# Kernel tuning notes

Hardware: AMD Instinct MI355X
Metric: run time of the kernel (lower is better)

The kernel has to match this reference:

```python
import jax, jax.numpy as jnp
import numpy as np

B, N, H = 32, 2048, 128
L4H = 4 * H  # concatenated (c0,h0,c1,h1) embedding dim


def _lstm_cell(x, c, h, Wx, Wh, b):
    g = x @ Wx + h @ Wh + b                      # [B,N,4H]
    i, f, gg, o = jnp.split(g, 4, axis=-1)
    c_new = jax.nn.sigmoid(f) * c + jax.nn.sigmoid(i) * jnp.tanh(gg)
    h_new = jax.nn.sigmoid(o) * jnp.tanh(c_new)
    return c_new, h_new


def setup_inputs() -> dict:
    key = jax.random.key(0)
    ks = jax.random.split(key, 20)
    s = 0.05
    inp = {
        'node_embeddings': jax.random.normal(ks[0], (B, N, H), jnp.float32),
        'c0': jax.random.normal(ks[1], (B, N, H), jnp.float32),
        'h0': jax.random.normal(ks[2], (B, N, H), jnp.float32),
        'c1': jax.random.normal(ks[3], (B, N, H), jnp.float32),
        'h1': jax.random.normal(ks[4], (B, N, H), jnp.float32),
        'instruction_pointer': jax.random.uniform(ks[5], (B, N), jnp.float32),
        'Wx0': s * jax.random.normal(ks[6], (H, 4 * H), jnp.float32),
        'Wh0': s * jax.random.normal(ks[7], (H, 4 * H), jnp.float32),
        'b0': jnp.zeros((4 * H,), jnp.float32),
        'Wx1': s * jax.random.normal(ks[8], (H, 4 * H), jnp.float32),
        'Wh1': s * jax.random.normal(ks[9], (H, 4 * H), jnp.float32),
        'b1': jnp.zeros((4 * H,), jnp.float32),
        'raise_W': s * jax.random.normal(ks[10], (L4H, 2), jnp.float32),
        'raise_b': jnp.zeros((2,), jnp.float32),
        'branch_W': s * jax.random.normal(ks[11], (L4H, 2), jnp.float32),
        'branch_b': jnp.zeros((2,), jnp.float32),
        'true_indexes': jax.random.randint(ks[12], (B, N), 0, N, jnp.int32),
        'false_indexes': jax.random.randint(ks[13], (B, N), 0, N, jnp.int32),
        'raise_indexes': jax.random.randint(ks[14], (B, N), 0, N, jnp.int32),
        'exit_node_indexes': jax.random.randint(ks[15], (B,), 0, N, jnp.int32),
        'raise_node_indexes': jax.random.randint(ks[16], (B,), 0, N, jnp.int32),
        'current_step': jnp.zeros((B,), jnp.int32),
        'step_limits': jax.random.randint(ks[17], (B,), 1, 100, jnp.int32),
    }
    return inp


def reference(node_embeddings, c0, h0, c1, h1, instruction_pointer,
              Wx0, Wh0, b0, Wx1, Wh1, b1, raise_W, raise_b, branch_W, branch_b,
              true_indexes, false_indexes, raise_indexes,
              exit_node_indexes, raise_node_indexes, current_step, step_limits):
    num_nodes = node_embeddings.shape[1]

    # --- execute: stacked 2-layer LSTM per node (vectorized over B,N) ---
    c0n, h0n = _lstm_cell(node_embeddings, c0, h0, Wx0, Wh0, b0)
    c1n, h1n = _lstm_cell(h0n, c1, h1, Wx1, Wh1, b1)
    old = (c0, h0, c1, h1)
    contrib = (c0n, h0n, c1n, h1n)

    # --- mask exit and raise nodes: keep old hidden state there ---
    node_ids = jnp.arange(num_nodes)[None, :]                  # [1,N]
    m_exit = node_ids == exit_node_indexes[:, None]            # [B,N]
    m_raise = node_ids == raise_node_indexes[:, None]          # [B,N]
    m_keep = (m_exit | m_raise)[..., None]                     # raise_in_ipagnn=True
    contrib = tuple(jnp.where(m_keep, o, c) for o, c in zip(old, contrib))

    # --- raise / branch decisions ---
    emb = jnp.concatenate(contrib, axis=-1)                    # [B,N,4H]
    raise_dec = jax.nn.softmax(emb @ raise_W + raise_b, axis=-1)
    raise_dec = jnp.where(m_exit[..., None], jnp.array([0.0, 1.0], raise_dec.dtype), raise_dec)
    branch_dec = jax.nn.softmax(emb @ branch_W + branch_b, axis=-1)

    p_raise = raise_dec[..., 0]
    p_noraise = raise_dec[..., 1]
    p_true = p_noraise * branch_dec[..., 0]
    p_false = p_noraise * branch_dec[..., 1]

    seg = jax.vmap(lambda d, i: jax.ops.segment_sum(d, i, num_segments=num_nodes))

    # --- instruction pointer update (scatter-add over soft edges) ---
    ip = instruction_pointer
    ip_new = (seg(p_raise * ip, raise_indexes)
              + seg(p_true * ip, true_indexes)
              + seg(p_false * ip, false_indexes))               # [B,N]

    # --- hidden-state aggregation, weighted by instruction pointer ---
    denom = (ip_new + 1e-7)[..., None]                          # [B,N,1]
    wr = (p_raise * ip)[..., None]
    wt = (p_true * ip)[..., None]
    wf = (p_false * ip)[..., None]
    agg = tuple((seg(hc * wr, raise_indexes)
                 + seg(hc * wt, true_indexes)
                 + seg(hc * wf, false_indexes)) / denom
                for hc in contrib)

    # --- keep old state if example already hit its step limit ---
    live = (current_step < step_limits)                         # [B]
    ip_fin = jnp.where(live[:, None], ip_new, ip)
    hid_fin = tuple(jnp.where(live[:, None, None], a, o) for a, o in zip(agg, old))

    # pack carry: (c0,h0,c1,h1) embedding + instruction pointer -> [B,N,4H+1]
    return jnp.concatenate(list(hid_fin) + [ip_fin[..., None]], axis=-1)
```

## Files before the change

kernel.cpp:

```cpp
#include <hip/hip_runtime.h>
#include <hip/hip_bf16.h>

constexpr int Bc  = 32;
constexpr int Nc  = 2048;
constexpr int Hc  = 128;
constexpr int H4c = 512;
constexpr int BNc = Bc * Nc;

typedef __attribute__((ext_vector_type(8))) short short8;
typedef __attribute__((ext_vector_type(4))) float f32x4;

__device__ __forceinline__ float sigf(float x) {
    x = fminf(15.f, fmaxf(-15.f, x));
    return 1.f / (1.f + __expf(-x));
}
__device__ __forceinline__ float tanh_(float x) {
    x = fminf(15.f, fmaxf(-15.f, x));
    float e = __expf(2.f * x);
    return (e - 1.f) / (e + 1.f);
}
__device__ __forceinline__ unsigned short bfu(float f) {
    union { float f; unsigned u; } a; a.f = f;
    unsigned u = a.u;
    return (unsigned short)((u + 0x7FFFu + ((u >> 16) & 1u)) >> 16);
}
__device__ __forceinline__ float bf2f(unsigned short u) {
    union { unsigned u; float f; } a; a.u = ((unsigned)u) << 16;
    return a.f;
}

__device__ __forceinline__ int a_off(int buf, int row, int byte) {
    return buf * 5120 + row * 80 + byte;
}
__device__ __forceinline__ int cs_off(int row, int unit) {
    return row * 512 + ((unit ^ (row & 7)) << 4);
}

__global__ __launch_bounds__(256) void prep_kernel(
    const float* __restrict__ Wx0, const float* __restrict__ Wh0,
    const float* __restrict__ Wx1, const float* __restrict__ Wh1,
    unsigned short* __restrict__ W0F, unsigned short* __restrict__ W1F)
{
    int idx = blockIdx.x * 256 + threadIdx.x;
    int ct = idx >> 9, ks = (idx >> 6) & 7, lane = idx & 63;
    int col = ct * 16 + (lane & 15);
    unsigned short* p0 = W0F + (size_t)idx * 8;
    unsigned short* p1 = W1F + (size_t)idx * 8;
    #pragma unroll
    for (int e = 0; e < 8; ++e) {
        int k = ks * 32 + (lane >> 4) * 8 + e;
        float v0 = (k < 128) ? Wx0[k * 512 + col] : Wh0[(k - 128) * 512 + col];
        float v1 = (k < 128) ? Wx1[k * 512 + col] : Wh1[(k - 128) * 512 + col];
        p0[e] = bfu(v0);
        p1[e] = bfu(v1);
    }
}

#define GEMM_CORE(WF, AB, STAGE)                                              \
    {                                                                         \
        STAGE(0, 0);                                                          \
        _Pragma("unroll")                                                     \
        for (int g = 0; g < 4; ++g)                                           \
            bn[g] = *(const short8*)(WF + ((size_t)((g * 8 + w) * 8 + 0) * 64 + l) * 8); \
        _Pragma("unroll")                                                     \
        for (int c = 0; c < 8; ++c) {                                         \
            __syncthreads();                                                  \
            short8 bc[4];                                                     \
            _Pragma("unroll")                                                 \
            for (int g = 0; g < 4; ++g) bc[g] = bn[g];                        \
            if (c < 7) {                                                      \
                STAGE(c + 1, (c + 1) & 1);                                    \
                _Pragma("unroll")                                             \
                for (int g = 0; g < 4; ++g)                                   \
                    bn[g] = *(const short8*)(WF + ((size_t)((g * 8 + w) * 8 + c + 1) * 64 + l) * 8); \
            }                                                                 \
            short8 a[4];                                                      \
            _Pragma("unroll")                                                 \
            for (int mt = 0; mt < 4; ++mt)                                    \
                a[mt] = *(const short8*)(AB + a_off(c & 1, mt * 16 + lr, lg * 16)); \
            _Pragma("unroll")                                                 \
            for (int mt = 0; mt < 4; ++mt)                                    \
                _Pragma("unroll")                                             \
                for (int g = 0; g < 4; ++g)                                   \
                    acc[mt][g] = __builtin_amdgcn_mfma_f32_16x16x32_bf16(     \
                        a[mt], bc[g], acc[mt][g], 0, 0, 0);                   \
        }                                                                     \
    }

__global__ __launch_bounds__(512, 4) void gemm0_kernel(
    const float* __restrict__ x_in,  const float* __restrict__ c0_in,
    const float* __restrict__ h0_in, const float* __restrict__ h1_in,
    const unsigned short* __restrict__ W0F, const float* __restrict__ b0,
    const int* __restrict__ exit_i, const int* __restrict__ raise_i,
    unsigned short* __restrict__ contrib, unsigned short* __restrict__ A1)
{
    __shared__ __align__(16) char Ab[10240];
    __shared__ __align__(16) char Cs[32768];

    const int t    = threadIdx.x;
    const int w    = t >> 6, l = t & 63, lr = l & 15, lg = l >> 4;
    const int row0 = blockIdx.x * 64;
    const int bidx = row0 >> 11;
    const int eb   = exit_i[bidx];
    const int rbn  = raise_i[bidx];
    const int j    = w * 16 + lr;

    const int srow = t >> 3, sfq = t & 7;
#define STAGE0(c, bi)                                                          \
    {                                                                          \
        const float* sp = ((c) < 4 ? x_in : h0_in)                             \
            + (size_t)(row0 + srow) * Hc + ((c) & 3) * 32 + sfq * 4;           \
        float4 v = *(const float4*)sp;                                         \
        ushort4 b4 = { bfu(v.x), bfu(v.y), bfu(v.z), bfu(v.w) };               \
        *(ushort4*)(Ab + a_off(bi, srow, sfq * 8)) = b4;                       \
    }

    f32x4 acc[4][4];
    #pragma unroll
    for (int g = 0; g < 4; ++g) {
        float bv = b0[g * 128 + j];
        f32x4 vv = {bv, bv, bv, bv};
        #pragma unroll
        for (int mt = 0; mt < 4; ++mt) acc[mt][g] = vv;
    }
    short8 bn[4];
    GEMM_CORE(W0F, Ab, STAGE0)

    unsigned hnp[4][4];
    #pragma unroll
    for (int mt = 0; mt < 4; ++mt) {
        #pragma unroll
        for (int rr = 0; rr < 4; ++rr) {
            const int row  = mt * 16 + lg * 4 + rr;
            const int grow = row0 + row;
            const int n    = grow & (Nc - 1);
            float cold = c0_in[(size_t)grow * Hc + j];
            float h0f  = h0_in[(size_t)grow * Hc + j];
            float h1f  = h1_in[(size_t)grow * Hc + j];
            float ig = sigf(acc[mt][0][rr]);
            float fg = sigf(acc[mt][1][rr]);
            float gv = tanh_(acc[mt][2][rr]);
            float og = sigf(acc[mt][3][rr]);
            float cn = fg * cold + ig * gv;
            float hn = og * tanh_(cn);
            const bool keep = (n == eb) || (n == rbn);
            *(unsigned short*)(Cs + cs_off(row, j >> 3) + (j & 7) * 2) =
                keep ? bfu(cold) : bfu(cn);
            *(unsigned short*)(Cs + cs_off(row, 16 + (j >> 3)) + (j & 7) * 2) =
                keep ? bfu(h0f) : bfu(hn);
            hnp[mt][rr] = (unsigned)bfu(hn) | ((unsigned)bfu(h1f) << 16);
        }
    }
    __syncthreads();
    #pragma unroll
    for (int i = 0; i < 4; ++i) {
        const int idx = i * 512 + t;
        const int r = idx >> 5, u = idx & 31;
        short8 v = *(const short8*)(Cs + cs_off(r, u));
        *(short8*)(contrib + (size_t)(row0 + r) * H4c + u * 8) = v;
    }
    __syncthreads();
    #pragma unroll
    for (int mt = 0; mt < 4; ++mt)
        #pragma unroll
        for (int rr = 0; rr < 4; ++rr) {
            const int row = mt * 16 + lg * 4 + rr;
            *(unsigned short*)(Cs + cs_off(row, j >> 3) + (j & 7) * 2) =
                (unsigned short)(hnp[mt][rr] & 0xFFFF);
            *(unsigned short*)(Cs + cs_off(row, 16 + (j >> 3)) + (j & 7) * 2) =
                (unsigned short)(hnp[mt][rr] >> 16);
        }
    __syncthreads();
    #pragma unroll
    for (int i = 0; i < 4; ++i) {
        const int idx = i * 512 + t;
        const int r = idx >> 5, u = idx & 31;
        short8 v = *(const short8*)(Cs + cs_off(r, u));
        *(short8*)(A1 + (size_t)(row0 + r) * 256 + u * 8) = v;
    }
#undef STAGE0
}

__global__ __launch_bounds__(512, 4) void gemm1_kernel(
    const unsigned short* __restrict__ A1, const float* __restrict__ c1_in,
    const unsigned short* __restrict__ W1F, const float* __restrict__ b1,
    const float* __restrict__ rW, const float* __restrict__ rbv,
    const float* __restrict__ bW, const float* __restrict__ bbv,
    const float* __restrict__ ip_in,
    const int* __restrict__ exit_i, const int* __restrict__ raise_i,
    unsigned short* __restrict__ contrib, float* __restrict__ w_all)
{
    __shared__ __align__(16) char Ab[10240];
    __shared__ __align__(16) char Cs[32768];

    const int t    = threadIdx.x;
    const int w    = t >> 6, l = t & 63, lr = l & 15, lg = l >> 4;
    const int row0 = blockIdx.x * 64;
    const int bidx = row0 >> 11;
    const int eb   = exit_i[bidx];
    const int rbn  = raise_i[bidx];
    const int j    = w * 16 + lr;

    const int srow = t >> 3, sfq = t & 7;
#define STAGE1(c, bi)                                                          \
    {                                                                          \
        ushort4 v = *(const ushort4*)(A1 + (size_t)(row0 + srow) * 256         \
                                      + (c) * 32 + sfq * 4);                   \
        *(ushort4*)(Ab + a_off(bi, srow, sfq * 8)) = v;                        \
    }

    f32x4 acc[4][4];
    #pragma unroll
    for (int g = 0; g < 4; ++g) {
        float bv = b1[g * 128 + j];
        f32x4 vv = {bv, bv, bv, bv};
        #pragma unroll
        for (int mt = 0; mt < 4; ++mt) acc[mt][g] = vv;
    }
    short8 bn[4];
    GEMM_CORE(W1F, Ab, STAGE1)

    #pragma unroll
    for (int mt = 0; mt < 4; ++mt) {
        #pragma unroll
        for (int rr = 0; rr < 4; ++rr) {
            const int row  = mt * 16 + lg * 4 + rr;
            const int grow = row0 + row;
            const int n    = grow & (Nc - 1);
            float cold = c1_in[(size_t)grow * Hc + j];
            unsigned short h1b = A1[(size_t)grow * 256 + 128 + j];
            float ig = sigf(acc[mt][0][rr]);
            float fg = sigf(acc[mt][1][rr]);
            float gv = tanh_(acc[mt][2][rr]);
            float og = sigf(acc[mt][3][rr]);
            float cn = fg * cold + ig * gv;
            float hn = og * tanh_(cn);
            const bool keep = (n == eb) || (n == rbn);
            *(unsigned short*)(Cs + cs_off(row, j >> 3) + (j & 7) * 2) =
                keep ? bfu(cold) : bfu(cn);
            *(unsigned short*)(Cs + cs_off(row, 16 + (j >> 3)) + (j & 7) * 2) =
                keep ? h1b : bfu(hn);
        }
    }
    __syncthreads();
    float* dw = (float*)Ab;
    if (t < 256) {
        ((float4*)dw)[t]       = ((const float4*)rW)[t];
        ((float4*)dw)[256 + t] = ((const float4*)bW)[t];
    }
    __syncthreads();
    #pragma unroll
    for (int i = 0; i < 4; ++i) {
        const int idx = i * 512 + t;
        const int r = idx >> 5, u = idx & 31;
        short8 v = *(const short8*)(Cs + cs_off(r, u));
        *(short8*)(contrib + (size_t)(row0 + r) * H4c + 256 + u * 8) = v;
    }

    {
        const int r8 = l >> 3, s = l & 7;
        const int row  = w * 8 + r8;
        const int grow = row0 + row;
        float pr0 = 0.f, pr1 = 0.f, pb0 = 0.f, pb1 = 0.f;
        #pragma unroll
        for (int cu = 0; cu < 8; ++cu) {
            short8 ev;
            if (s < 4)
                ev = *(const short8*)(contrib + (size_t)grow * H4c + s * 64 + cu * 8);
            else
                ev = *(const short8*)(Cs + cs_off(row, (s - 4) * 8 + cu));
            const int col0 = s * 64 + cu * 8;
            const float4* rp = (const float4*)(dw + col0 * 2);
            const float4* bp = (const float4*)(dw + 1024 + col0 * 2);
            #pragma unroll
            for (int q = 0; q < 4; ++q) {
                float4 rv = rp[q], bv = bp[q];
                float e0 = bf2f((unsigned short)ev[q * 2]);
                float e1 = bf2f((unsigned short)ev[q * 2 + 1]);
                pr0 += e0 * rv.x + e1 * rv.z;
                pr1 += e0 * rv.y + e1 * rv.w;
                pb0 += e0 * bv.x + e1 * bv.z;
                pb1 += e0 * bv.y + e1 * bv.w;
            }
        }
        #pragma unroll
        for (int m = 1; m < 8; m <<= 1) {
            pr0 += __shfl_xor(pr0, m);
            pr1 += __shfl_xor(pr1, m);
            pb0 += __shfl_xor(pb0, m);
            pb1 += __shfl_xor(pb1, m);
        }
        if (s == 0) {
            const int n = grow & (Nc - 1);
            float r0v = pr0 + rbv[0], r1v = pr1 + rbv[1];
            float m  = fmaxf(r0v, r1v);
            float z0 = __expf(r0v - m), z1 = __expf(r1v - m);
            float inv = 1.f / (z0 + z1);
            float praise = z0 * inv, pno = z1 * inv;
            if (n == eb) { praise = 0.f; pno = 1.f; }
            float q0 = pb0 + bbv[0], q1 = pb1 + bbv[1];
            float mm = fmaxf(q0, q1);
            float y0 = __expf(q0 - mm), y1 = __expf(q1 - mm);
            float binv = 1.f / (y0 + y1);
            float ipv = ip_in[grow];
            w_all[grow]            = praise * ipv;
            w_all[BNc + grow]      = pno * y0 * binv * ipv;
            w_all[2 * BNc + grow]  = pno * y1 * binv * ipv;
        }
    }
#undef STAGE1
}

__global__ __launch_bounds__(256) void build_kernel(
    const int* __restrict__ t_idx, const int* __restrict__ f_idx,
    const int* __restrict__ r_idx, int* __restrict__ head, int* __restrict__ nxt)
{
    const int row  = blockIdx.x * 256 + threadIdx.x;
    const int base = (row >> 11) << 11;
    const int e0 = row * 4;
    int o;
    o = atomicExch(&head[base + r_idx[row]], e0);     nxt[e0]     = o;
    o = atomicExch(&head[base + t_idx[row]], e0 + 1); nxt[e0 + 1] = o;
    o = atomicExch(&head[base + f_idx[row]], e0 + 2); nxt[e0 + 2] = o;
}

__global__ __launch_bounds__(256) void gather_kernel(
    const unsigned short* __restrict__ contrib, const float* __restrict__ w_all,
    const int* __restrict__ head, const int* __restrict__ nxt,
    const float* __restrict__ c0_in, const float* __restrict__ h0_in,
    const float* __restrict__ c1_in, const float* __restrict__ h1_in,
    const float* __restrict__ ip_in,
    const int* __restrict__ cstep, const int* __restrict__ slim,
    float* __restrict__ out)
{
    const int gtid = blockIdx.x * 256 + threadIdx.x;
    const int wid  = gtid >> 6;
    const int l    = gtid & 63;
    const int bidx = wid >> 11;

    float acc[8] = {0.f, 0.f, 0.f, 0.f, 0.f, 0.f, 0.f, 0.f};
    float ipsum = 0.f;

    int e = head[wid];
    while (e >= 0) {
        const int src = e >> 2;
        const float w = w_all[(e & 3) * BNc + src];
        const unsigned short* crow = contrib + (size_t)src * 512;
        #pragma unroll
        for (int q = 0; q < 8; ++q) acc[q] += w * bf2f(crow[q * 64 + l]);
        ipsum += w;
        e = nxt[e];
    }

    const bool live = cstep[bidx] < slim[bidx];
    float* orow = out + (size_t)wid * 513;
    if (live) {
        const float inv = 1.f / (ipsum + 1e-7f);
        #pragma unroll
        for (int q = 0; q < 8; ++q) orow[q * 64 + l] = acc[q] * inv;
        if (l == 0) orow[512] = ipsum;
    } else {
        #pragma unroll
        for (int q = 0; q < 8; ++q) {
            const int off = (q & 1) * 64 + l;
            const float* p = (q >> 1) == 0 ? c0_in : (q >> 1) == 1 ? h0_in
                           : (q >> 1) == 2 ? c1_in : h1_in;
            orow[q * 64 + l] = p[(size_t)wid * Hc + off];
        }
        if (l == 0) orow[512] = ip_in[wid];
    }
}

extern "C" void kernel_launch(void* const* d_in, const int* in_sizes, int n_in,
                              void* d_out, int out_size, void* d_ws, size_t ws_size,
                              hipStream_t stream) {
    const float* x     = (const float*)d_in[0];
    const float* c0    = (const float*)d_in[1];
    const float* h0    = (const float*)d_in[2];
    const float* c1    = (const float*)d_in[3];
    const float* h1    = (const float*)d_in[4];
    const float* ip    = (const float*)d_in[5];
    const float* Wx0   = (const float*)d_in[6];
    const float* Wh0   = (const float*)d_in[7];
    const float* b0    = (const float*)d_in[8];
    const float* Wx1   = (const float*)d_in[9];
    const float* Wh1   = (const float*)d_in[10];
    const float* b1    = (const float*)d_in[11];
    const float* rW    = (const float*)d_in[12];
    const float* rb    = (const float*)d_in[13];
    const float* bW    = (const float*)d_in[14];
    const float* bb    = (const float*)d_in[15];
    const int* t_idx   = (const int*)d_in[16];
    const int* f_idx   = (const int*)d_in[17];
    const int* r_idx   = (const int*)d_in[18];
    const int* exit_i  = (const int*)d_in[19];
    const int* raise_i = (const int*)d_in[20];
    const int* cstep   = (const int*)d_in[21];
    const int* slim    = (const int*)d_in[22];
    float* out = (float*)d_out;

    unsigned short* contrib = (unsigned short*)d_ws;
    unsigned short* A1  = contrib + (size_t)BNc * 512;
    unsigned short* W0F = A1 + (size_t)BNc * 256;
    unsigned short* W1F = W0F + 512 * 256;
    float* w_all = (float*)(W1F + 512 * 256);
    int*   head  = (int*)(w_all + 3 * (size_t)BNc);
    int*   nxt   = head + BNc;

    hipMemsetAsync(head, 0xFF, BNc * sizeof(int), stream);

    prep_kernel<<<64, 256, 0, stream>>>(Wx0, Wh0, Wx1, Wh1, W0F, W1F);
    gemm0_kernel<<<BNc / 64, 512, 0, stream>>>(x, c0, h0, h1, W0F, b0,
                                               exit_i, raise_i, contrib, A1);
    gemm1_kernel<<<BNc / 64, 512, 0, stream>>>(A1, c1, W1F, b1,
                                               rW, rb, bW, bb, ip,
                                               exit_i, raise_i, contrib, w_all);
    build_kernel<<<BNc / 256, 256, 0, stream>>>(t_idx, f_idx, r_idx, head, nxt);
    gather_kernel<<<BNc / 4, 256, 0, stream>>>(contrib, w_all, head, nxt,
                                               c0, h0, c1, h1, ip, cstep, slim, out);
}
```

Baseline: 205.0 us.

## Write layer-1 input in MFMA fragment layout and stream it directly in gemm1

gemm0 now writes the intermediate A1 buffer pre-swizzled into MFMA A-fragment order, so gemm1 loads its operands straight from global memory into registers without LDS staging or per-chunk barriers. Conversions to bf16 use the packed v_cvt_pk_bf16_f32 instruction, with lane-pair shuffles so each LDS store writes 32 bits. The clamp on sigmoid/tanh inputs is dropped, h0/h1 are read only when the keep condition holds, and the head weights are loaded into LDS at kernel start. The risk is lower latency hiding in gemm1's unstaged loads, and the unclamped tanh form relies on exp overflow behaving correctly.

```diff
diff --git a/kernel.cpp b/kernel.cpp
--- a/kernel.cpp
+++ b/kernel.cpp
@@ -10,15 +10,9 @@
 typedef __attribute__((ext_vector_type(8))) short short8;
 typedef __attribute__((ext_vector_type(4))) float f32x4;
 
-__device__ __forceinline__ float sigf(float x) {
-    x = fminf(15.f, fmaxf(-15.f, x));
-    return 1.f / (1.f + __expf(-x));
-}
-__device__ __forceinline__ float tanh_(float x) {
-    x = fminf(15.f, fmaxf(-15.f, x));
-    float e = __expf(2.f * x);
-    return (e - 1.f) / (e + 1.f);
-}
+__device__ __forceinline__ float sigf(float x)  { return 1.f / (1.f + __expf(-x)); }
+__device__ __forceinline__ float tanh_(float x) { return 1.f - 2.f / (__expf(2.f * x) + 1.f); }
+
 __device__ __forceinline__ unsigned short bfu(float f) {
     union { float f; unsigned u; } a; a.f = f;
     unsigned u = a.u;
@@ -27,6 +21,11 @@
 __device__ __forceinline__ float bf2f(unsigned short u) {
     union { unsigned u; float f; } a; a.u = ((unsigned)u) << 16;
     return a.f;
+}
+__device__ __forceinline__ unsigned cvtpk(float lo, float hi) {
+    unsigned r;
+    asm("v_cvt_pk_bf16_f32 %0, %1, %2" : "=v"(r) : "v"(lo), "v"(hi));
+    return r;
 }
 
 __device__ __forceinline__ int a_off(int buf, int row, int byte) {
@@ -56,43 +55,12 @@
     }
 }
 
-#define GEMM_CORE(WF, AB, STAGE)                                              \
-    {                                                                         \
-        STAGE(0, 0);                                                          \
-        _Pragma("unroll")                                                     \
-        for (int g = 0; g < 4; ++g)                                           \
-            bn[g] = *(const short8*)(WF + ((size_t)((g * 8 + w) * 8 + 0) * 64 + l) * 8); \
-        _Pragma("unroll")                                                     \
-        for (int c = 0; c < 8; ++c) {                                         \
-            __syncthreads();                                                  \
-            short8 bc[4];                                                     \
-            _Pragma("unroll")                                                 \
-            for (int g = 0; g < 4; ++g) bc[g] = bn[g];                        \
-            if (c < 7) {                                                      \
-                STAGE(c + 1, (c + 1) & 1);                                    \
-                _Pragma("unroll")                                             \
-                for (int g = 0; g < 4; ++g)                                   \
-                    bn[g] = *(const short8*)(WF + ((size_t)((g * 8 + w) * 8 + c + 1) * 64 + l) * 8); \
-            }                                                                 \
-            short8 a[4];                                                      \
-            _Pragma("unroll")                                                 \
-            for (int mt = 0; mt < 4; ++mt)                                    \
-                a[mt] = *(const short8*)(AB + a_off(c & 1, mt * 16 + lr, lg * 16)); \
-            _Pragma("unroll")                                                 \
-            for (int mt = 0; mt < 4; ++mt)                                    \
-                _Pragma("unroll")                                             \
-                for (int g = 0; g < 4; ++g)                                   \
-                    acc[mt][g] = __builtin_amdgcn_mfma_f32_16x16x32_bf16(     \
-                        a[mt], bc[g], acc[mt][g], 0, 0, 0);                   \
-        }                                                                     \
-    }
-
 __global__ __launch_bounds__(512, 4) void gemm0_kernel(
     const float* __restrict__ x_in,  const float* __restrict__ c0_in,
     const float* __restrict__ h0_in, const float* __restrict__ h1_in,
     const unsigned short* __restrict__ W0F, const float* __restrict__ b0,
     const int* __restrict__ exit_i, const int* __restrict__ raise_i,
-    unsigned short* __restrict__ contrib, unsigned short* __restrict__ A1)
+    unsigned short* __restrict__ contrib, unsigned short* __restrict__ A1F)
 {
     __shared__ __align__(16) char Ab[10240];
     __shared__ __align__(16) char Cs[32768];
@@ -111,8 +79,8 @@
         const float* sp = ((c) < 4 ? x_in : h0_in)                             \
             + (size_t)(row0 + srow) * Hc + ((c) & 3) * 32 + sfq * 4;           \
         float4 v = *(const float4*)sp;                                         \
-        ushort4 b4 = { bfu(v.x), bfu(v.y), bfu(v.z), bfu(v.w) };               \
-        *(ushort4*)(Ab + a_off(bi, srow, sfq * 8)) = b4;                       \
+        uint2 b2 = { cvtpk(v.x, v.y), cvtpk(v.z, v.w) };                       \
+        *(uint2*)(Ab + a_off(bi, srow, sfq * 8)) = b2;                         \
     }
 
     f32x4 acc[4][4];
@@ -123,8 +91,35 @@
         #pragma unroll
         for (int mt = 0; mt < 4; ++mt) acc[mt][g] = vv;
     }
+
+    STAGE0(0, 0);
     short8 bn[4];
-    GEMM_CORE(W0F, Ab, STAGE0)
+    #pragma unroll
+    for (int g = 0; g < 4; ++g)
+        bn[g] = *(const short8*)(W0F + ((size_t)((g * 8 + w) * 8) * 64 + l) * 8);
+    #pragma unroll
+    for (int c = 0; c < 8; ++c) {
+        __syncthreads();
+        short8 bc[4];
+        #pragma unroll
+        for (int g = 0; g < 4; ++g) bc[g] = bn[g];
+        if (c < 7) {
+            STAGE0(c + 1, (c + 1) & 1);
+            #pragma unroll
+            for (int g = 0; g < 4; ++g)
+                bn[g] = *(const short8*)(W0F + ((size_t)((g * 8 + w) * 8 + c + 1) * 64 + l) * 8);
+        }
+        short8 a[4];
+        #pragma unroll
+        for (int mt = 0; mt < 4; ++mt)
+            a[mt] = *(const short8*)(Ab + a_off(c & 1, mt * 16 + lr, lg * 16));
+        #pragma unroll
+        for (int mt = 0; mt < 4; ++mt)
+            #pragma unroll
+            for (int g = 0; g < 4; ++g)
+                acc[mt][g] = __builtin_amdgcn_mfma_f32_16x16x32_bf16(
+                    a[mt], bc[g], acc[mt][g], 0, 0, 0);
+    }
 
     unsigned hnp[4][4];
     #pragma unroll
@@ -135,7 +130,6 @@
             const int grow = row0 + row;
             const int n    = grow & (Nc - 1);
             float cold = c0_in[(size_t)grow * Hc + j];
-            float h0f  = h0_in[(size_t)grow * Hc + j];
             float h1f  = h1_in[(size_t)grow * Hc + j];
             float ig = sigf(acc[mt][0][rr]);
             float fg = sigf(acc[mt][1][rr]);
@@ -144,11 +138,16 @@
             float cn = fg * cold + ig * gv;
             float hn = og * tanh_(cn);
             const bool keep = (n == eb) || (n == rbn);
-            *(unsigned short*)(Cs + cs_off(row, j >> 3) + (j & 7) * 2) =
-                keep ? bfu(cold) : bfu(cn);
-            *(unsigned short*)(Cs + cs_off(row, 16 + (j >> 3)) + (j & 7) * 2) =
-                keep ? bfu(h0f) : bfu(hn);
-            hnp[mt][rr] = (unsigned)bfu(hn) | ((unsigned)bfu(h1f) << 16);
+            float cw = keep ? cold : cn;
+            float hw = hn;
+            if (keep) hw = h0_in[(size_t)grow * Hc + j];
+            float cwn = __shfl_xor(cw, 1);
+            float hwn = __shfl_xor(hw, 1);
+            if (!(lr & 1)) {
+                *(unsigned*)(Cs + cs_off(row, j >> 3) + (j & 7) * 2)        = cvtpk(cw, cwn);
+                *(unsigned*)(Cs + cs_off(row, 16 + (j >> 3)) + (j & 7) * 2) = cvtpk(hw, hwn);
+            }
+            hnp[mt][rr] = cvtpk(hn, h1f);
         }
     }
     __syncthreads();
@@ -165,24 +164,32 @@
         #pragma unroll
         for (int rr = 0; rr < 4; ++rr) {
             const int row = mt * 16 + lg * 4 + rr;
-            *(unsigned short*)(Cs + cs_off(row, j >> 3) + (j & 7) * 2) =
-                (unsigned short)(hnp[mt][rr] & 0xFFFF);
-            *(unsigned short*)(Cs + cs_off(row, 16 + (j >> 3)) + (j & 7) * 2) =
-                (unsigned short)(hnp[mt][rr] >> 16);
+            unsigned pn = __shfl_xor(hnp[mt][rr], 1);
+            if (!(lr & 1)) {
+                unsigned h0d = (hnp[mt][rr] & 0xFFFFu) | (pn << 16);
+                unsigned h1d = (hnp[mt][rr] >> 16) | (pn & 0xFFFF0000u);
+                *(unsigned*)(Cs + cs_off(row, j >> 3) + (j & 7) * 2)        = h0d;
+                *(unsigned*)(Cs + cs_off(row, 16 + (j >> 3)) + (j & 7) * 2) = h1d;
+            }
         }
     __syncthreads();
     #pragma unroll
     for (int i = 0; i < 4; ++i) {
-        const int idx = i * 512 + t;
-        const int r = idx >> 5, u = idx & 31;
-        short8 v = *(const short8*)(Cs + cs_off(r, u));
-        *(short8*)(A1 + (size_t)(row0 + r) * 256 + u * 8) = v;
+        const int idx  = i * 512 + t;
+        const int frag = idx >> 6;
+        const int lane = idx & 63;
+        const int mt = frag >> 3, ks = frag & 7;
+        const int row  = mt * 16 + (lane & 15);
+        const int unit = ks * 4 + (lane >> 4);
+        short8 v = *(const short8*)(Cs + cs_off(row, unit));
+        *(short8*)(A1F + (((size_t)blockIdx.x * 32 + frag) << 9) + (size_t)lane * 8) = v;
     }
 #undef STAGE0
 }
 
 __global__ __launch_bounds__(512, 4) void gemm1_kernel(
-    const unsigned short* __restrict__ A1, const float* __restrict__ c1_in,
+    const unsigned short* __restrict__ A1F, const float* __restrict__ c1_in,
+    const float* __restrict__ h1_in,
     const unsigned short* __restrict__ W1F, const float* __restrict__ b1,
     const float* __restrict__ rW, const float* __restrict__ rbv,
     const float* __restrict__ bW, const float* __restrict__ bbv,
@@ -190,8 +197,8 @@
     const int* __restrict__ exit_i, const int* __restrict__ raise_i,
     unsigned short* __restrict__ contrib, float* __restrict__ w_all)
 {
-    __shared__ __align__(16) char Ab[10240];
     __shared__ __align__(16) char Cs[32768];
+    __shared__ __align__(16) float dw[2048];
 
     const int t    = threadIdx.x;
     const int w    = t >> 6, l = t & 63, lr = l & 15, lg = l >> 4;
@@ -201,12 +208,9 @@
     const int rbn  = raise_i[bidx];
     const int j    = w * 16 + lr;
 
-    const int srow = t >> 3, sfq = t & 7;
-#define STAGE1(c, bi)                                                          \
-    {                                                                          \
-        ushort4 v = *(const ushort4*)(A1 + (size_t)(row0 + srow) * 256         \
-                                      + (c) * 32 + sfq * 4);                   \
-        *(ushort4*)(Ab + a_off(bi, srow, sfq * 8)) = v;                        \
+    if (t < 256) {
+        ((float4*)dw)[t]       = ((const float4*)rW)[t];
+        ((float4*)dw)[256 + t] = ((const float4*)bW)[t];
     }
 
     f32x4 acc[4][4];
@@ -217,8 +221,24 @@
         #pragma unroll
         for (int mt = 0; mt < 4; ++mt) acc[mt][g] = vv;
     }
-    short8 bn[4];
-    GEMM_CORE(W1F, Ab, STAGE1)
+
+    const unsigned short* Af = A1F + ((size_t)blockIdx.x * 32 << 9);
+    #pragma unroll
+    for (int ks = 0; ks < 8; ++ks) {
+        short8 a[4], b[4];
+        #pragma unroll
+        for (int mt = 0; mt < 4; ++mt)
+            a[mt] = *(const short8*)(Af + (((size_t)(mt * 8 + ks)) << 9) + (size_t)l * 8);
+        #pragma unroll
+        for (int g = 0; g < 4; ++g)
+            b[g] = *(const short8*)(W1F + ((size_t)((g * 8 + w) * 8 + ks) * 64 + l) * 8);
+        #pragma unroll
+        for (int mt = 0; mt < 4; ++mt)
+            #pragma unroll
+            for (int g = 0; g < 4; ++g)
+                acc[mt][g] = __builtin_amdgcn_mfma_f32_16x16x32_bf16(
+                    a[mt], b[g], acc[mt][g], 0, 0, 0);
+    }
 
     #pragma unroll
     for (int mt = 0; mt < 4; ++mt) {
@@ -228,7 +248,6 @@
             const int grow = row0 + row;
             const int n    = grow & (Nc - 1);
             float cold = c1_in[(size_t)grow * Hc + j];
-            unsigned short h1b = A1[(size_t)grow * 256 + 128 + j];
             float ig = sigf(acc[mt][0][rr]);
             float fg = sigf(acc[mt][1][rr]);
             float gv = tanh_(acc[mt][2][rr]);
@@ -236,19 +255,19 @@
             float cn = fg * cold + ig * gv;
             float hn = og * tanh_(cn);
             const bool keep = (n == eb) || (n == rbn);
-            *(unsigned short*)(Cs + cs_off(row, j >> 3) + (j & 7) * 2) =
-                keep ? bfu(cold) : bfu(cn);
-            *(unsigned short*)(Cs + cs_off(row, 16 + (j >> 3)) + (j & 7) * 2) =
-                keep ? h1b : bfu(hn);
+            float cw = keep ? cold : cn;
+            float hw = hn;
+            if (keep) hw = h1_in[(size_t)grow * Hc + j];
+            float cwn = __shfl_xor(cw, 1);
+            float hwn = __shfl_xor(hw, 1);
+            if (!(lr & 1)) {
+                *(unsigned*)(Cs + cs_off(row, j >> 3) + (j & 7) * 2)        = cvtpk(cw, cwn);
+                *(unsigned*)(Cs + cs_off(row, 16 + (j >> 3)) + (j & 7) * 2) = cvtpk(hw, hwn);
+            }
         }
     }
     __syncthreads();
-    float* dw = (float*)Ab;
-    if (t < 256) {
-        ((float4*)dw)[t]       = ((const float4*)rW)[t];
-        ((float4*)dw)[256 + t] = ((const float4*)bW)[t];
-    }
-    __syncthreads();
+
     #pragma unroll
     for (int i = 0; i < 4; ++i) {
         const int idx = i * 512 + t;
@@ -308,7 +327,6 @@
             w_all[2 * BNc + grow]  = pno * y1 * binv * ipv;
         }
     }
-#undef STAGE1
 }
 
 __global__ __launch_bounds__(256) void build_kernel(
@@ -400,8 +418,8 @@
     float* out = (float*)d_out;
 
     unsigned short* contrib = (unsigned short*)d_ws;
-    unsigned short* A1  = contrib + (size_t)BNc * 512;
-    unsigned short* W0F = A1 + (size_t)BNc * 256;
+    unsigned short* A1F = contrib + (size_t)BNc * 512;
+    unsigned short* W0F = A1F + (size_t)BNc * 256;
     unsigned short* W1F = W0F + 512 * 256;
     float* w_all = (float*)(W1F + 512 * 256);
     int*   head  = (int*)(w_all + 3 * (size_t)BNc);
@@ -411,8 +429,8 @@
 
     prep_kernel<<<64, 256, 0, stream>>>(Wx0, Wh0, Wx1, Wh1, W0F, W1F);
     gemm0_kernel<<<BNc / 64, 512, 0, stream>>>(x, c0, h0, h1, W0F, b0,
-                                               exit_i, raise_i, contrib, A1);
-    gemm1_kernel<<<BNc / 64, 512, 0, stream>>>(A1, c1, W1F, b1,
+                                               exit_i, raise_i, contrib, A1F);
+    gemm1_kernel<<<BNc / 64, 512, 0, stream>>>(A1F, c1, h1, W1F, b1,
                                                rW, rb, bW, bb, ip,
                                                exit_i, raise_i, contrib, w_all);
     build_kernel<<<BNc / 256, 256, 0, stream>>>(t_idx, f_idx, r_idx, head, nxt);
```

Result: slower. 214.3 us (+4.5%).
